# Kernel optimization log

Hardware: AMD Instinct MI355X
Metric: run time of the kernel (lower is better)

Reference implementation:

```python
import jax, jax.numpy as jnp
import numpy as np

B, T, C, W, H, HID = 64, 1024, 256, 28, 28, 512


def setup_inputs() -> dict:
    key = jax.random.key(0)
    k1, k2, k3, k4, k5, k6 = jax.random.split(key, 6)
    text = jax.random.normal(k1, (B, T), dtype=jnp.float32)
    vision = jax.random.normal(k2, (B, C, W, H), dtype=jnp.float32)
    s1 = 1.0 / np.sqrt(T + C)
    s2 = 1.0 / np.sqrt(HID)
    W1 = jax.random.uniform(k3, (T + C, HID), jnp.float32, -s1, s1)
    b1 = jax.random.uniform(k4, (HID,), jnp.float32, -s1, s1)
    W2 = jax.random.uniform(k5, (HID, 1), jnp.float32, -s2, s2)
    b2 = jax.random.uniform(k6, (1,), jnp.float32, -s2, s2)
    return {"text": text, "vision": vision, "W1": W1, "b1": b1, "W2": W2, "b2": b2}


def reference(text, vision, W1, b1, W2, b2):
    b, c, w, h = vision.shape
    p = w * h
    # pixels in (i*height + j) order, matching the torch double loop / view
    pixels = vision.transpose(0, 2, 3, 1).reshape(b, p, c)  # (B, P, C)
    text_b = jnp.broadcast_to(text[:, None, :], (b, p, text.shape[1]))
    feat = jnp.concatenate([text_b, pixels], axis=-1)        # (B, P, T+C)
    hidden = jax.nn.relu(jnp.einsum("bpf,fh->bph", feat, W1) + b1)
    scores = (jnp.einsum("bph,ho->bpo", hidden, W2) + b2)[..., 0]  # (B, P)
    weights = jax.nn.softmax(scores, axis=1)                 # (B, P)
    pooled = jnp.einsum("bpc,bp->bc", pixels, weights)       # (B, C)
    return jnp.concatenate([pooled, text], axis=1)           # (B, C+T)
```

## Files before the change

kernel.cpp:

```cpp
#include <hip/hip_runtime.h>

#define BB  64
#define TT  1024
#define CC  256
#define PP  784
#define HID 512
#define FF  1280

typedef float v4f __attribute__((ext_vector_type(4)));
typedef short v8s __attribute__((ext_vector_type(8)));

__device__ inline unsigned int bf16_rne_bits(float x) {
    unsigned int u = __float_as_uint(x);
    unsigned int r = u + 0x7FFFu + ((u >> 16) & 1u);
    return r & 0xFFFF0000u;
}

__global__ __launch_bounds__(256) void k_w1t(const float* __restrict__ W1,
                                             unsigned short* __restrict__ w1t_hi,
                                             unsigned short* __restrict__ w1t_lo) {
    const int id = blockIdx.x * 256 + threadIdx.x;
    const int h  = id & 511;
    const int cg = id >> 9;
    const int cstep = cg >> 2, g = cg & 3;
    const float* W1v = W1 + (size_t)TT * HID;
    unsigned int hw[4], lw[4];
    #pragma unroll
    for (int k = 0; k < 4; ++k) {
        const int c0 = cstep * 32 + g * 8 + 2 * k;
        float x0 = W1v[(size_t)c0 * HID + h];
        float x1 = W1v[(size_t)(c0 + 1) * HID + h];
        unsigned int h0 = bf16_rne_bits(x0), h1 = bf16_rne_bits(x1);
        unsigned int l0 = bf16_rne_bits(x0 - __uint_as_float(h0));
        unsigned int l1 = bf16_rne_bits(x1 - __uint_as_float(h1));
        hw[k] = (h0 >> 16) | (h1 & 0xFFFF0000u);
        lw[k] = (l0 >> 16) | (l1 & 0xFFFF0000u);
    }
    const size_t eoff = ((size_t)((h >> 8) * 8 + cstep) * 256 + (h & 255)) * 32 + g * 8;
    *(int4*)(&w1t_hi[eoff]) = make_int4(hw[0], hw[1], hw[2], hw[3]);
    *(int4*)(&w1t_lo[eoff]) = make_int4(lw[0], lw[1], lw[2], lw[3]);
}

__global__ __launch_bounds__(512) void k_text_gemm(const float* __restrict__ text,
                                                   const float* __restrict__ W1,
                                                   float* __restrict__ tbp) {
    const int b  = blockIdx.x;
    const int ks = blockIdx.y;
    const int t  = threadIdx.x;
    __shared__ float st[256];
    if (t < 256) st[t] = text[b * TT + ks * 256 + t];
    __syncthreads();
    float acc = 0.f;
    const float* wp = W1 + (size_t)(ks * 256) * HID + t;
    #pragma unroll 4
    for (int k = 0; k < 256; ++k)
        acc = fmaf(st[k], wp[(size_t)k * HID], acc);
    tbp[(b * 4 + ks) * HID + t] = acc;
}

__global__ __launch_bounds__(256, 2) void k_vision_mfma(
        const float* __restrict__ vision,
        const unsigned short* __restrict__ w1t_hi,
        const unsigned short* __restrict__ w1t_lo,
        const float* __restrict__ b1,
        const float* __restrict__ W2,
        const float* __restrict__ tbp,
        float* __restrict__ scores) {
    const int ptile = blockIdx.x;
    const int hh    = blockIdx.y;
    const int b     = blockIdx.z;
    const int tid   = threadIdx.x;
    const int lane  = tid & 63;
    const int w     = tid >> 6;
    const int l15   = lane & 15, lg = lane >> 4;

    __shared__ int4 lds4[47104 / 16];
    char* lds = (char*)lds4;

    v4f acc[7][4];
    #pragma unroll
    for (int m = 0; m < 7; ++m)
        #pragma unroll
        for (int n = 0; n < 4; ++n) acc[m][n] = (v4f){0.f, 0.f, 0.f, 0.f};

    const size_t vbase = (size_t)b * (CC * PP) + ptile * 112;

    for (int ks = 0; ks < 8; ++ks) {
        {
            const size_t boff = (size_t)(hh * 8 + ks) * 8192;
            const int4* srcH = (const int4*)(w1t_hi + boff);
            const int4* srcL = (const int4*)(w1t_lo + boff);
            int4* dstH = (int4*)(lds + 0);
            int4* dstL = (int4*)(lds + 16384);
            #pragma unroll
            for (int r = 0; r < 4; ++r) {
                dstH[r * 256 + tid] = srcH[r * 256 + tid];
                dstL[r * 256 + tid] = srcL[r * 256 + tid];
            }
        }
        if (tid < 224) {
            const int px    = tid >> 1;
            const int chalf = tid & 1;
            float xv[16];
            #pragma unroll
            for (int j = 0; j < 16; ++j) {
                const int c = ks * 32 + chalf * 16 + j;
                xv[j] = vision[vbase + (size_t)c * PP + px];
            }
            unsigned int hw[8], lw[8];
            #pragma unroll
            for (int k = 0; k < 8; ++k) {
                unsigned int h0 = bf16_rne_bits(xv[2 * k]);
                unsigned int h1 = bf16_rne_bits(xv[2 * k + 1]);
                unsigned int l0 = bf16_rne_bits(xv[2 * k] - __uint_as_float(h0));
                unsigned int l1 = bf16_rne_bits(xv[2 * k + 1] - __uint_as_float(h1));
                hw[k] = (h0 >> 16) | (h1 & 0xFFFF0000u);
                lw[k] = (l0 >> 16) | (l1 & 0xFFFF0000u);
            }
            int4* ah = (int4*)(lds + 32768) + (px * 4 + chalf * 2);
            int4* al = (int4*)(lds + 39936) + (px * 4 + chalf * 2);
            ah[0] = make_int4(hw[0], hw[1], hw[2], hw[3]);
            ah[1] = make_int4(hw[4], hw[5], hw[6], hw[7]);
            al[0] = make_int4(lw[0], lw[1], lw[2], lw[3]);
            al[1] = make_int4(lw[4], lw[5], lw[6], lw[7]);
        }
        __syncthreads();
        v8s ahf[7], alf[7];
        #pragma unroll
        for (int m = 0; m < 7; ++m) {
            const int row = m * 16 + l15;
            ahf[m] = *(const v8s*)(lds + 32768 + (row * 4 + lg) * 16);
            alf[m] = *(const v8s*)(lds + 39936 + (row * 4 + lg) * 16);
        }
        #pragma unroll
        for (int n = 0; n < 4; ++n) {
            const int hrow = w * 64 + n * 16 + l15;
            const v8s bh = *(const v8s*)(lds + 0     + (hrow * 4 + lg) * 16);
            const v8s bl = *(const v8s*)(lds + 16384 + (hrow * 4 + lg) * 16);
            #pragma unroll
            for (int m = 0; m < 7; ++m) {
                acc[m][n] = __builtin_amdgcn_mfma_f32_16x16x32_bf16(ahf[m], bh, acc[m][n], 0, 0, 0);
                acc[m][n] = __builtin_amdgcn_mfma_f32_16x16x32_bf16(ahf[m], bl, acc[m][n], 0, 0, 0);
                acc[m][n] = __builtin_amdgcn_mfma_f32_16x16x32_bf16(alf[m], bh, acc[m][n], 0, 0, 0);
            }
        }
        __syncthreads();
    }

    float tbn[4], w2n[4];
    #pragma unroll
    for (int n = 0; n < 4; ++n) {
        const int hglob = hh * 256 + w * 64 + n * 16 + l15;
        const float* tp = tbp + (size_t)b * 4 * HID + hglob;
        tbn[n] = b1[hglob] + tp[0] + tp[HID] + tp[2 * HID] + tp[3 * HID];
        w2n[n] = W2[hglob];
    }
    const int px0 = ptile * 112 + lg * 4;
    #pragma unroll
    for (int m = 0; m < 7; ++m) {
        #pragma unroll
        for (int r = 0; r < 4; ++r) {
            float s = 0.f;
            #pragma unroll
            for (int n = 0; n < 4; ++n)
                s += fmaxf(acc[m][n][r] + tbn[n], 0.f) * w2n[n];
            s += __shfl_xor(s, 1, 64);
            s += __shfl_xor(s, 2, 64);
            s += __shfl_xor(s, 4, 64);
            s += __shfl_xor(s, 8, 64);
            if (l15 == 0)
                atomicAdd(&scores[b * PP + px0 + m * 16 + r], s);
        }
    }
}

__global__ __launch_bounds__(256) void k_softmax_copy(float* __restrict__ sw,
                                                      const float* __restrict__ text,
                                                      float* __restrict__ out) {
    const int b   = blockIdx.x;
    const int tid = threadIdx.x;
    const int lane = tid & 63, wid = tid >> 6;
    __shared__ float red[4];

    float v[4]; int cnt = 0;
    float m = -3.4e38f;
    for (int p = tid; p < PP; p += 256) { v[cnt] = sw[b * PP + p]; m = fmaxf(m, v[cnt]); ++cnt; }
    #pragma unroll
    for (int off = 32; off > 0; off >>= 1) m = fmaxf(m, __shfl_xor(m, off, 64));
    if (lane == 0) red[wid] = m;
    __syncthreads();
    m = fmaxf(fmaxf(red[0], red[1]), fmaxf(red[2], red[3]));
    __syncthreads();

    float ssum = 0.f;
    for (int i = 0; i < cnt; ++i) { v[i] = expf(v[i] - m); ssum += v[i]; }
    #pragma unroll
    for (int off = 32; off > 0; off >>= 1) ssum += __shfl_xor(ssum, off, 64);
    if (lane == 0) red[wid] = ssum;
    __syncthreads();
    const float inv = 1.f / (red[0] + red[1] + red[2] + red[3]);

    cnt = 0;
    for (int p = tid; p < PP; p += 256) sw[b * PP + p] = v[cnt++] * inv;

    for (int j = tid; j < TT; j += 256) out[b * FF + CC + j] = text[b * TT + j];
}

__global__ __launch_bounds__(256) void k_pool(const float* __restrict__ vision,
                                              const float* __restrict__ wts,
                                              float* __restrict__ out) {
    const int cg = blockIdx.x;
    const int b  = blockIdx.y;
    const int tid = threadIdx.x, lane = tid & 63, wid = tid >> 6;
    __shared__ float wl[PP];
    {
        const int i = tid * 4;
        if (i < PP) *(float4*)&wl[i] = *(const float4*)&wts[b * PP + i];
    }
    __syncthreads();
    #pragma unroll
    for (int ci = 0; ci < 16; ++ci) {
        const int c = cg * 64 + wid * 16 + ci;
        const float* vr = vision + (size_t)b * (CC * PP) + (size_t)c * PP;
        float acc = 0.f;
        #pragma unroll
        for (int k = 0; k < 4; ++k) {
            const int p4 = (lane + 64 * k) * 4;
            if (p4 < PP) {
                const float4 vv = *(const float4*)(vr + p4);
                const float4 ww = *(const float4*)&wl[p4];
                acc = fmaf(vv.x, ww.x, acc);
                acc = fmaf(vv.y, ww.y, acc);
                acc = fmaf(vv.z, ww.z, acc);
                acc = fmaf(vv.w, ww.w, acc);
            }
        }
        #pragma unroll
        for (int off = 32; off > 0; off >>= 1) acc += __shfl_xor(acc, off, 64);
        if (lane == 0) out[b * FF + c] = acc;
    }
}

extern "C" void kernel_launch(void* const* d_in, const int* in_sizes, int n_in,
                              void* d_out, int out_size, void* d_ws, size_t ws_size,
                              hipStream_t stream) {
    const float* text   = (const float*)d_in[0];
    const float* vision = (const float*)d_in[1];
    const float* W1     = (const float*)d_in[2];
    const float* b1     = (const float*)d_in[3];
    const float* W2     = (const float*)d_in[4];
    float* out = (float*)d_out;

    float* tbp = (float*)d_ws;
    float* sw  = tbp + BB * 4 * HID;
    unsigned short* w1t_hi = (unsigned short*)(sw + BB * PP);
    unsigned short* w1t_lo = w1t_hi + 131072;

    k_w1t        <<<64, 256, 0, stream>>>(W1, w1t_hi, w1t_lo);
    k_text_gemm  <<<dim3(BB, 4), 512, 0, stream>>>(text, W1, tbp);
    hipMemsetAsync(sw, 0, BB * PP * sizeof(float), stream);
    k_vision_mfma<<<dim3(7, 2, BB), 256, 0, stream>>>(vision, w1t_hi, w1t_lo,
                                                      b1, W2, tbp, sw);
    k_softmax_copy<<<BB, 256, 0, stream>>>(sw, text, out);
    k_pool       <<<dim3(4, BB), 256, 0, stream>>>(vision, sw, out);
}
```

Baseline: 185.0 us.

## Double-buffer vision tile in LDS, read W1 fragments from global, widen text/pool grids

The vision MFMA kernel now double-buffers the bf16-split vision tile in LDS. It prefetches the next channel slice into registers while the current one feeds the MFMAs, and the W1 B-fragments are read directly from global memory (and cache) instead of being staged through LDS. LDS per block shrinks to about 28 KB and one barrier per K-step is removed, at the cost of extra global loads of W1 per wave and more register pressure. Separately, the text GEMM is split into 8 K-chunks instead of 4 and the pool kernel uses 8 channel groups instead of 4, which raises block counts for those small kernels.

```diff
diff --git a/kernel.cpp b/kernel.cpp
--- a/kernel.cpp
+++ b/kernel.cpp
@@ -47,15 +47,15 @@
     const int b  = blockIdx.x;
     const int ks = blockIdx.y;
     const int t  = threadIdx.x;
-    __shared__ float st[256];
-    if (t < 256) st[t] = text[b * TT + ks * 256 + t];
+    __shared__ float st[128];
+    if (t < 128) st[t] = text[b * TT + ks * 128 + t];
     __syncthreads();
     float acc = 0.f;
-    const float* wp = W1 + (size_t)(ks * 256) * HID + t;
+    const float* wp = W1 + (size_t)(ks * 128) * HID + t;
     #pragma unroll 4
-    for (int k = 0; k < 256; ++k)
+    for (int k = 0; k < 128; ++k)
         acc = fmaf(st[k], wp[(size_t)k * HID], acc);
-    tbp[(b * 4 + ks) * HID + t] = acc;
+    tbp[(b * 8 + ks) * HID + t] = acc;
 }
 
 __global__ __launch_bounds__(256, 2) void k_vision_mfma(
@@ -74,8 +74,7 @@
     const int w     = tid >> 6;
     const int l15   = lane & 15, lg = lane >> 4;
 
-    __shared__ int4 lds4[47104 / 16];
-    char* lds = (char*)lds4;
+    __shared__ int4 lds4[2][896];
 
     v4f acc[7][4];
     #pragma unroll
@@ -84,66 +83,61 @@
         for (int n = 0; n < 4; ++n) acc[m][n] = (v4f){0.f, 0.f, 0.f, 0.f};
 
     const size_t vbase = (size_t)b * (CC * PP) + ptile * 112;
+    const int spx = tid >> 1, sch = tid & 1;
+
+    float xv[16];
+    #define A_LOAD(KS) do { if (tid < 224) { \
+        _Pragma("unroll") for (int j = 0; j < 16; ++j) { \
+            const int c_ = (KS) * 32 + sch * 16 + j; \
+            xv[j] = vision[vbase + (size_t)c_ * PP + spx]; } } } while (0)
+
+    #define A_WRITE(BUF) do { if (tid < 224) { \
+        unsigned int hw[8], lw[8]; \
+        _Pragma("unroll") for (int q = 0; q < 8; ++q) { \
+            unsigned int h0 = bf16_rne_bits(xv[2 * q]); \
+            unsigned int h1 = bf16_rne_bits(xv[2 * q + 1]); \
+            unsigned int l0 = bf16_rne_bits(xv[2 * q] - __uint_as_float(h0)); \
+            unsigned int l1 = bf16_rne_bits(xv[2 * q + 1] - __uint_as_float(h1)); \
+            hw[q] = (h0 >> 16) | (h1 & 0xFFFF0000u); \
+            lw[q] = (l0 >> 16) | (l1 & 0xFFFF0000u); } \
+        int4* ah = (int4*)(&lds4[BUF][0]) + (spx * 4 + sch * 2); \
+        int4* al = (int4*)((char*)&lds4[BUF][0] + 7168) + (spx * 4 + sch * 2); \
+        ah[0] = make_int4(hw[0], hw[1], hw[2], hw[3]); \
+        ah[1] = make_int4(hw[4], hw[5], hw[6], hw[7]); \
+        al[0] = make_int4(lw[0], lw[1], lw[2], lw[3]); \
+        al[1] = make_int4(lw[4], lw[5], lw[6], lw[7]); } } while (0)
+
+    A_LOAD(0);
+    A_WRITE(0);
+    __syncthreads();
+
+    const int bfr = ((w * 64 + l15) * 4 + lg) * 8;
 
     for (int ks = 0; ks < 8; ++ks) {
-        {
-            const size_t boff = (size_t)(hh * 8 + ks) * 8192;
-            const int4* srcH = (const int4*)(w1t_hi + boff);
-            const int4* srcL = (const int4*)(w1t_lo + boff);
-            int4* dstH = (int4*)(lds + 0);
-            int4* dstL = (int4*)(lds + 16384);
+        const int cur = ks & 1;
+        if (ks < 7) A_LOAD(ks + 1);
+        const unsigned short* bkh = w1t_hi + (size_t)(hh * 8 + ks) * 8192 + bfr;
+        const unsigned short* bkl = w1t_lo + (size_t)(hh * 8 + ks) * 8192 + bfr;
+        v8s bh[4], bl[4];
+        #pragma unroll
+        for (int n = 0; n < 4; ++n) {
+            bh[n] = *(const v8s*)(bkh + n * 512);
+            bl[n] = *(const v8s*)(bkl + n * 512);
+        }
+        const char* abuf = (const char*)&lds4[cur][0];
+        #pragma unroll
+        for (int m = 0; m < 7; ++m) {
+            const int fo = ((m * 16 + l15) * 4 + lg) * 16;
+            const v8s ah = *(const v8s*)(abuf + fo);
+            const v8s al = *(const v8s*)(abuf + 7168 + fo);
             #pragma unroll
-            for (int r = 0; r < 4; ++r) {
-                dstH[r * 256 + tid] = srcH[r * 256 + tid];
-                dstL[r * 256 + tid] = srcL[r * 256 + tid];
+            for (int n = 0; n < 4; ++n) {
+                acc[m][n] = __builtin_amdgcn_mfma_f32_16x16x32_bf16(ah, bh[n], acc[m][n], 0, 0, 0);
+                acc[m][n] = __builtin_amdgcn_mfma_f32_16x16x32_bf16(ah, bl[n], acc[m][n], 0, 0, 0);
+                acc[m][n] = __builtin_amdgcn_mfma_f32_16x16x32_bf16(al, bh[n], acc[m][n], 0, 0, 0);
             }
         }
-        if (tid < 224) {
-            const int px    = tid >> 1;
-            const int chalf = tid & 1;
-            float xv[16];
-            #pragma unroll
-            for (int j = 0; j < 16; ++j) {
-                const int c = ks * 32 + chalf * 16 + j;
-                xv[j] = vision[vbase + (size_t)c * PP + px];
-            }
-            unsigned int hw[8], lw[8];
-            #pragma unroll
-            for (int k = 0; k < 8; ++k) {
-                unsigned int h0 = bf16_rne_bits(xv[2 * k]);
-                unsigned int h1 = bf16_rne_bits(xv[2 * k + 1]);
-                unsigned int l0 = bf16_rne_bits(xv[2 * k] - __uint_as_float(h0));
-                unsigned int l1 = bf16_rne_bits(xv[2 * k + 1] - __uint_as_float(h1));
-                hw[k] = (h0 >> 16) | (h1 & 0xFFFF0000u);
-                lw[k] = (l0 >> 16) | (l1 & 0xFFFF0000u);
-            }
-            int4* ah = (int4*)(lds + 32768) + (px * 4 + chalf * 2);
-            int4* al = (int4*)(lds + 39936) + (px * 4 + chalf * 2);
-            ah[0] = make_int4(hw[0], hw[1], hw[2], hw[3]);
-            ah[1] = make_int4(hw[4], hw[5], hw[6], hw[7]);
-            al[0] = make_int4(lw[0], lw[1], lw[2], lw[3]);
-            al[1] = make_int4(lw[4], lw[5], lw[6], lw[7]);
-        }
-        __syncthreads();
-        v8s ahf[7], alf[7];
-        #pragma unroll
-        for (int m = 0; m < 7; ++m) {
-            const int row = m * 16 + l15;
-            ahf[m] = *(const v8s*)(lds + 32768 + (row * 4 + lg) * 16);
-            alf[m] = *(const v8s*)(lds + 39936 + (row * 4 + lg) * 16);
-        }
-        #pragma unroll
-        for (int n = 0; n < 4; ++n) {
-            const int hrow = w * 64 + n * 16 + l15;
-            const v8s bh = *(const v8s*)(lds + 0     + (hrow * 4 + lg) * 16);
-            const v8s bl = *(const v8s*)(lds + 16384 + (hrow * 4 + lg) * 16);
-            #pragma unroll
-            for (int m = 0; m < 7; ++m) {
-                acc[m][n] = __builtin_amdgcn_mfma_f32_16x16x32_bf16(ahf[m], bh, acc[m][n], 0, 0, 0);
-                acc[m][n] = __builtin_amdgcn_mfma_f32_16x16x32_bf16(ahf[m], bl, acc[m][n], 0, 0, 0);
-                acc[m][n] = __builtin_amdgcn_mfma_f32_16x16x32_bf16(alf[m], bh, acc[m][n], 0, 0, 0);
-            }
-        }
+        if (ks < 7) A_WRITE(cur ^ 1);
         __syncthreads();
     }
 
@@ -151,8 +145,11 @@
     #pragma unroll
     for (int n = 0; n < 4; ++n) {
         const int hglob = hh * 256 + w * 64 + n * 16 + l15;
-        const float* tp = tbp + (size_t)b * 4 * HID + hglob;
-        tbn[n] = b1[hglob] + tp[0] + tp[HID] + tp[2 * HID] + tp[3 * HID];
+        const float* tp = tbp + (size_t)b * 8 * HID + hglob;
+        float tv = b1[hglob];
+        #pragma unroll
+        for (int q = 0; q < 8; ++q) tv += tp[q * HID];
+        tbn[n] = tv;
         w2n[n] = W2[hglob];
     }
     const int px0 = ptile * 112 + lg * 4;
@@ -172,6 +169,8 @@
                 atomicAdd(&scores[b * PP + px0 + m * 16 + r], s);
         }
     }
+    #undef A_LOAD
+    #undef A_WRITE
 }
 
 __global__ __launch_bounds__(256) void k_softmax_copy(float* __restrict__ sw,
@@ -219,8 +218,8 @@
     }
     __syncthreads();
     #pragma unroll
-    for (int ci = 0; ci < 16; ++ci) {
-        const int c = cg * 64 + wid * 16 + ci;
+    for (int ci = 0; ci < 8; ++ci) {
+        const int c = cg * 32 + wid * 8 + ci;
         const float* vr = vision + (size_t)b * (CC * PP) + (size_t)c * PP;
         float acc = 0.f;
         #pragma unroll
@@ -252,15 +251,15 @@
     float* out = (float*)d_out;
 
     float* tbp = (float*)d_ws;
-    float* sw  = tbp + BB * 4 * HID;
+    float* sw  = tbp + BB * 8 * HID;
     unsigned short* w1t_hi = (unsigned short*)(sw + BB * PP);
     unsigned short* w1t_lo = w1t_hi + 131072;
 
     k_w1t        <<<64, 256, 0, stream>>>(W1, w1t_hi, w1t_lo);
-    k_text_gemm  <<<dim3(BB, 4), 512, 0, stream>>>(text, W1, tbp);
+    k_text_gemm  <<<dim3(BB, 8), 512, 0, stream>>>(text, W1, tbp);
     hipMemsetAsync(sw, 0, BB * PP * sizeof(float), stream);
     k_vision_mfma<<<dim3(7, 2, BB), 256, 0, stream>>>(vision, w1t_hi, w1t_lo,
                                                       b1, W2, tbp, sw);
     k_softmax_copy<<<BB, 256, 0, stream>>>(sw, text, out);
-    k_pool       <<<dim3(4, BB), 256, 0, stream>>>(vision, sw, out);
-}
+    k_pool       <<<dim3(8, BB), 256, 0, stream>>>(vision, sw, out);
+}
```

After: 175.0 us. 5.4% less time.
